# Performance work log

Measured on AMD Instinct MI355X. Metric: run time of the kernel, lower is better.

Reference implementation:

```python
import jax, jax.numpy as jnp
import numpy as np


def setup_inputs() -> dict:
    key = jax.random.key(0)
    k1, k2, k3, k4 = jax.random.split(key, 4)
    C, R = 64, 8  # channels, reduced = channels // 8
    B, D, H, W = 2, 16, 16, 16
    x = jax.random.normal(k1, (B, C, D, H, W), dtype=jnp.float32)
    # 1x1x1 Conv3d kernels are plain [out_ch, in_ch] matrices (no bias)
    Wq = jax.random.normal(k2, (R, C), dtype=jnp.float32) * (C ** -0.5)
    Wk = jax.random.normal(k3, (R, C), dtype=jnp.float32) * (C ** -0.5)
    Wv = jax.random.normal(k4, (C, C), dtype=jnp.float32) * (C ** -0.5)
    gamma = jnp.ones((1,), dtype=jnp.float32) * 0.5  # nonzero so output depends on attention
    return {"x": x, "Wq": Wq, "Wk": Wk, "Wv": Wv, "gamma": gamma}


def reference(x, Wq, Wk, Wv, gamma):
    b, c, d, h, w = x.shape
    n = d * h * w
    xf = x.astype(jnp.float32).reshape(b, c, n)        # [b, c, n]
    q = jnp.einsum('rc,bcn->bnr', Wq, xf)              # [b, n, r]
    k = jnp.einsum('rc,bcn->brn', Wk, xf)              # [b, r, n]
    scale = q.shape[-1] ** -0.5
    attn = jax.nn.softmax(jnp.einsum('bnr,brm->bnm', q, k) * scale, axis=-1)  # [b, n_q, n_k]
    v = jnp.einsum('oc,bcn->bon', Wv, xf)              # [b, c, n]
    # out = value @ attn^T : out[b,c,q] = sum_k v[b,c,k] * attn[b,q,k]
    out = jnp.einsum('bck,bqk->bcq', v, attn).reshape(b, c, d, h, w)
    return x + gamma.astype(x.dtype) * out.astype(x.dtype)
```

## Files before the change

kernel.cpp:

```cpp
#include <hip/hip_runtime.h>
#include <math.h>

#define BB 2
#define CC 64
#define NN 4096
#define SCALE 0.35355339059327373f

typedef _Float16 f16x8 __attribute__((ext_vector_type(8)));
typedef _Float16 f16x4 __attribute__((ext_vector_type(4)));
typedef float f32x4 __attribute__((ext_vector_type(4)));

__global__ __launch_bounds__(256) void proj_kernel(
    const float* __restrict__ x, const float* __restrict__ Wq,
    const float* __restrict__ Wk, const float* __restrict__ Wv,
    _Float16* __restrict__ qh, _Float16* __restrict__ kh,
    _Float16* __restrict__ vph)
{
    const int t = (int)blockIdx.x * 256 + (int)threadIdx.x;
    const int grp = t >> 13;
    const int p = t & 8191;
    const int b = p >> 12;
    const int n = p & (NN - 1);
    const float* xp = x + (size_t)b * CC * NN + n;

    float xc[CC];
#pragma unroll
    for (int c = 0; c < CC; ++c) xc[c] = xp[(size_t)c * NN];

    const float* W = (grp == 0) ? Wq : (grp == 1) ? Wk
                                     : (Wv + (size_t)(grp - 2) * 8 * CC);
    float a[8];
#pragma unroll
    for (int j = 0; j < 8; ++j) a[j] = 0.f;
#pragma unroll
    for (int c = 0; c < CC; ++c) {
        const float xv = xc[c];
#pragma unroll
        for (int j = 0; j < 8; ++j)
            a[j] = fmaf(W[j * CC + c], xv, a[j]);
    }
    if (grp == 0) {
        f16x8 o;
#pragma unroll
        for (int j = 0; j < 8; ++j) o[j] = (_Float16)(a[j] * SCALE);
        *(f16x8*)(qh + ((size_t)b * NN + n) * 8) = o;
    } else if (grp == 1) {
        f16x8 o;
#pragma unroll
        for (int j = 0; j < 8; ++j) o[j] = (_Float16)a[j];
        *(f16x8*)(kh + ((size_t)b * NN + n) * 8) = o;
    } else {
        const int c0 = (grp - 2) * 8;
        _Float16* vb = vph + ((size_t)(b * 512 + (n >> 3)) * CC + c0) * 8 + (n & 7);
#pragma unroll
        for (int j = 0; j < 8; ++j) vb[j * 8] = (_Float16)a[j];
    }
}

__global__ __launch_bounds__(512) void attn_kernel(
    const _Float16* __restrict__ qh, const _Float16* __restrict__ kh,
    const _Float16* __restrict__ vph, const float* __restrict__ x,
    const float* __restrict__ gamma, float* __restrict__ out)
{
    const int tid = (int)threadIdx.x;
    const int wid = tid >> 6;
    const int lane = tid & 63;
    const int lg = lane >> 4;
    const int lc = lane & 15;
    const int qi = (int)blockIdx.x & 255;
    const int b  = (int)blockIdx.x >> 8;
    const int q0 = qi * 16;

    __shared__ float sm_acc[8 * 64 * 17];
    __shared__ float sm_m[8][16];
    __shared__ float sm_l[8][16];

    const f16x8 zf = {};
    const f32x4 z4 = {};

    f16x8 qfrag = zf;
    if (lg == 0)
        qfrag = *(const f16x8*)(qh + ((size_t)b * NN + q0 + lc) * 8);

    float m = -1e30f, l = 0.f;
    f32x4 acc0 = z4, acc1 = z4, acc2 = z4, acc3 = z4;

    const _Float16* khb = kh + (size_t)b * NN * 8;
    const _Float16* vpb = vph + (size_t)b * 512 * CC * 8;
    const int kbase = wid * 512;

#pragma unroll 4
    for (int ch = 0; ch < 16; ++ch) {
        const int k0 = kbase + ch * 32;

        f16x8 kf0 = zf, kf1 = zf;
        if (lg == 0) {
            kf0 = *(const f16x8*)(khb + (size_t)(k0 + lc) * 8);
            kf1 = *(const f16x8*)(khb + (size_t)(k0 + 16 + lc) * 8);
        }
        const _Float16* vg = vpb + ((size_t)((k0 >> 3) + lg) * CC) * 8;
        f16x8 v0 = *(const f16x8*)(vg + (0 * 16 + lc) * 8);
        f16x8 v1 = *(const f16x8*)(vg + (1 * 16 + lc) * 8);
        f16x8 v2 = *(const f16x8*)(vg + (2 * 16 + lc) * 8);
        f16x8 v3 = *(const f16x8*)(vg + (3 * 16 + lc) * 8);

        f32x4 s0 = __builtin_amdgcn_mfma_f32_16x16x32_f16(kf0, qfrag, z4, 0, 0, 0);
        f32x4 s1 = __builtin_amdgcn_mfma_f32_16x16x32_f16(kf1, qfrag, z4, 0, 0, 0);

        float cm = fmaxf(fmaxf(fmaxf(s0[0], s0[1]), fmaxf(s0[2], s0[3])),
                         fmaxf(fmaxf(s1[0], s1[1]), fmaxf(s1[2], s1[3])));
        cm = fmaxf(cm, __shfl_xor(cm, 16));
        cm = fmaxf(cm, __shfl_xor(cm, 32));

        if (!__all(cm <= m)) {
            const float mnew = fmaxf(m, cm);
            const float alpha = __expf(m - mnew);
            m = mnew;
            l *= alpha;
            acc0 *= alpha; acc1 *= alpha; acc2 *= alpha; acc3 *= alpha;
        }

        float pr[8];
        float ls = 0.f;
#pragma unroll
        for (int v = 0; v < 4; ++v) { pr[v]     = __expf(s0[v] - m); ls += pr[v]; }
#pragma unroll
        for (int v = 0; v < 4; ++v) { pr[4 + v] = __expf(s1[v] - m); ls += pr[4 + v]; }
        ls += __shfl_xor(ls, 16);
        ls += __shfl_xor(ls, 32);
        l += ls;

        union { f16x4 h; unsigned u[2]; } P0, P1;
#pragma unroll
        for (int v = 0; v < 4; ++v) {
            P0.h[v] = (_Float16)pr[v];
            P1.h[v] = (_Float16)pr[4 + v];
        }
        const int sA = (((2 * lg) & 3) << 4) + lc;
        const int sB = (((2 * lg + 1) & 3) << 4) + lc;
        const unsigned t00 = __shfl(P0.u[0], sA), t01 = __shfl(P0.u[1], sA);
        const unsigned t10 = __shfl(P1.u[0], sA), t11 = __shfl(P1.u[1], sA);
        const unsigned u00 = __shfl(P0.u[0], sB), u01 = __shfl(P0.u[1], sB);
        const unsigned u10 = __shfl(P1.u[0], sB), u11 = __shfl(P1.u[1], sB);
        const bool hi = (lg & 2) != 0;
        union { unsigned u[4]; f16x8 v; } PF;
        PF.u[0] = hi ? t10 : t00;
        PF.u[1] = hi ? t11 : t01;
        PF.u[2] = hi ? u10 : u00;
        PF.u[3] = hi ? u11 : u01;

        acc0 = __builtin_amdgcn_mfma_f32_16x16x32_f16(v0, PF.v, acc0, 0, 0, 0);
        acc1 = __builtin_amdgcn_mfma_f32_16x16x32_f16(v1, PF.v, acc1, 0, 0, 0);
        acc2 = __builtin_amdgcn_mfma_f32_16x16x32_f16(v2, PF.v, acc2, 0, 0, 0);
        acc3 = __builtin_amdgcn_mfma_f32_16x16x32_f16(v3, PF.v, acc3, 0, 0, 0);
    }

    if (lane < 16) { sm_m[wid][lc] = m; sm_l[wid][lc] = l; }
    {
        float* sa = sm_acc + (size_t)wid * 64 * 17 + lc;
#pragma unroll
        for (int v = 0; v < 4; ++v) {
            sa[(0 * 16 + lg * 4 + v) * 17] = acc0[v];
            sa[(1 * 16 + lg * 4 + v) * 17] = acc1[v];
            sa[(2 * 16 + lg * 4 + v) * 17] = acc2[v];
            sa[(3 * 16 + lg * 4 + v) * 17] = acc3[v];
        }
    }
    __syncthreads();

    {
        const int c = tid >> 3;
        const int qb2 = (tid & 7) * 2;
        const float g = gamma[0];
#pragma unroll
        for (int dq = 0; dq < 2; ++dq) {
            const int q = qb2 + dq;
            float M = sm_m[0][q];
#pragma unroll
            for (int w = 1; w < 8; ++w) M = fmaxf(M, sm_m[w][q]);
            float L = 0.f, O = 0.f;
#pragma unroll
            for (int w = 0; w < 8; ++w) {
                const float e = __expf(sm_m[w][q] - M);
                L = fmaf(sm_l[w][q], e, L);
                O = fmaf(sm_acc[(w * 64 + c) * 17 + q], e, O);
            }
            const size_t oi = (size_t)b * CC * NN + (size_t)c * NN + q0 + q;
            out[oi] = fmaf(g, O / L, x[oi]);
        }
    }
}

extern "C" void kernel_launch(void* const* d_in, const int* in_sizes, int n_in,
                              void* d_out, int out_size, void* d_ws, size_t ws_size,
                              hipStream_t stream)
{
    const float* x     = (const float*)d_in[0];
    const float* Wq    = (const float*)d_in[1];
    const float* Wk    = (const float*)d_in[2];
    const float* Wv    = (const float*)d_in[3];
    const float* gamma = (const float*)d_in[4];
    float* out = (float*)d_out;

    char* ws = (char*)d_ws;
    _Float16* qh  = (_Float16*)ws;
    _Float16* kh  = qh + (size_t)BB * NN * 8;
    _Float16* vph = kh + (size_t)BB * NN * 8;

    hipLaunchKernelGGL(proj_kernel, dim3(320), dim3(256), 0, stream,
                       x, Wq, Wk, Wv, qh, kh, vph);
    hipLaunchKernelGGL(attn_kernel, dim3(BB * 256), dim3(512), 0, stream,
                       qh, kh, vph, x, gamma, out);
}
```

Before: 90.53 us.

## Fuse projection and attention via grid barrier, apply Wv after attention

After: 235.4 us. +160.0%, slower.

```diff
diff --git a/kernel.cpp b/kernel.cpp
--- a/kernel.cpp
+++ b/kernel.cpp
@@ -4,76 +4,89 @@
 #define BB 2
 #define CC 64
 #define NN 4096
+#define NBLK 512
 #define SCALE 0.35355339059327373f
 
 typedef _Float16 f16x8 __attribute__((ext_vector_type(8)));
 typedef _Float16 f16x4 __attribute__((ext_vector_type(4)));
 typedef float f32x4 __attribute__((ext_vector_type(4)));
 
-__global__ __launch_bounds__(256) void proj_kernel(
+union H2U { _Float16 h; unsigned short u; };
+static __device__ inline unsigned short f2h_bits(float f) {
+    H2U c; c.h = (_Float16)f; return c.u;
+}
+
+__global__ __launch_bounds__(512, 4) void fused_kernel(
     const float* __restrict__ x, const float* __restrict__ Wq,
     const float* __restrict__ Wk, const float* __restrict__ Wv,
-    _Float16* __restrict__ qh, _Float16* __restrict__ kh,
-    _Float16* __restrict__ vph)
-{
-    const int t = (int)blockIdx.x * 256 + (int)threadIdx.x;
-    const int grp = t >> 13;
-    const int p = t & 8191;
-    const int b = p >> 12;
-    const int n = p & (NN - 1);
-    const float* xp = x + (size_t)b * CC * NN + n;
-
-    float xc[CC];
-#pragma unroll
-    for (int c = 0; c < CC; ++c) xc[c] = xp[(size_t)c * NN];
-
-    const float* W = (grp == 0) ? Wq : (grp == 1) ? Wk
-                                     : (Wv + (size_t)(grp - 2) * 8 * CC);
-    float a[8];
-#pragma unroll
-    for (int j = 0; j < 8; ++j) a[j] = 0.f;
-#pragma unroll
-    for (int c = 0; c < CC; ++c) {
-        const float xv = xc[c];
-#pragma unroll
-        for (int j = 0; j < 8; ++j)
-            a[j] = fmaf(W[j * CC + c], xv, a[j]);
-    }
-    if (grp == 0) {
-        f16x8 o;
-#pragma unroll
-        for (int j = 0; j < 8; ++j) o[j] = (_Float16)(a[j] * SCALE);
-        *(f16x8*)(qh + ((size_t)b * NN + n) * 8) = o;
-    } else if (grp == 1) {
-        f16x8 o;
-#pragma unroll
-        for (int j = 0; j < 8; ++j) o[j] = (_Float16)a[j];
-        *(f16x8*)(kh + ((size_t)b * NN + n) * 8) = o;
-    } else {
-        const int c0 = (grp - 2) * 8;
-        _Float16* vb = vph + ((size_t)(b * 512 + (n >> 3)) * CC + c0) * 8 + (n & 7);
-#pragma unroll
-        for (int j = 0; j < 8; ++j) vb[j * 8] = (_Float16)a[j];
-    }
-}
-
-__global__ __launch_bounds__(512) void attn_kernel(
-    const _Float16* __restrict__ qh, const _Float16* __restrict__ kh,
-    const _Float16* __restrict__ vph, const float* __restrict__ x,
-    const float* __restrict__ gamma, float* __restrict__ out)
+    const float* __restrict__ gamma, float* __restrict__ out,
+    unsigned* __restrict__ ctr, _Float16* __restrict__ qh,
+    _Float16* __restrict__ kh, _Float16* __restrict__ xh)
 {
     const int tid = (int)threadIdx.x;
+    const int bid = (int)blockIdx.x;
+    const int gt = bid * 512 + tid;
+
+    __shared__ float sm_acc[8 * 64 * 17];
+    __shared__ float sm_m[8][16];
+    __shared__ float sm_l[8][16];
+    __shared__ float zm[64][16];
+
+    {
+        const float2 v = ((const float2*)x)[gt];
+        ushort2 h; h.x = f2h_bits(v.x); h.y = f2h_bits(v.y);
+        ((ushort2*)xh)[gt] = h;
+    }
+    if (gt < BB * NN) {
+        const int b = gt >> 12;
+        const int n = gt & (NN - 1);
+        const float* xp = x + (size_t)b * CC * NN + n;
+        float xc[CC];
+#pragma unroll
+        for (int c = 0; c < CC; ++c) xc[c] = xp[(size_t)c * NN];
+        float aq[8], ak[8];
+#pragma unroll
+        for (int r = 0; r < 8; ++r) { aq[r] = 0.f; ak[r] = 0.f; }
+#pragma unroll
+        for (int c = 0; c < CC; ++c) {
+            const float xv = xc[c];
+#pragma unroll
+            for (int r = 0; r < 8; ++r) {
+                aq[r] = fmaf(Wq[r * CC + c], xv, aq[r]);
+                ak[r] = fmaf(Wk[r * CC + c], xv, ak[r]);
+            }
+        }
+        f16x8 oq, ok;
+#pragma unroll
+        for (int r = 0; r < 8; ++r) {
+            oq[r] = (_Float16)(aq[r] * SCALE);
+            ok[r] = (_Float16)ak[r];
+        }
+        *(f16x8*)(qh + (size_t)gt * 8) = oq;
+        *(f16x8*)(kh + (size_t)gt * 8) = ok;
+    }
+
+    __threadfence();
+    __syncthreads();
+    if (tid == 0) {
+        atomicAdd(ctr, 1u);
+        int guard = 0;
+        while (__hip_atomic_load(ctr, __ATOMIC_ACQUIRE,
+                                 __HIP_MEMORY_SCOPE_AGENT) < (unsigned)NBLK &&
+               guard < (1 << 20)) {
+            __builtin_amdgcn_s_sleep(8);
+            ++guard;
+        }
+    }
+    __syncthreads();
+
     const int wid = tid >> 6;
     const int lane = tid & 63;
     const int lg = lane >> 4;
     const int lc = lane & 15;
-    const int qi = (int)blockIdx.x & 255;
-    const int b  = (int)blockIdx.x >> 8;
+    const int b  = bid & 1;
+    const int qi = bid >> 1;
     const int q0 = qi * 16;
-
-    __shared__ float sm_acc[8 * 64 * 17];
-    __shared__ float sm_m[8][16];
-    __shared__ float sm_l[8][16];
 
     const f16x8 zf = {};
     const f32x4 z4 = {};
@@ -86,7 +99,7 @@
     f32x4 acc0 = z4, acc1 = z4, acc2 = z4, acc3 = z4;
 
     const _Float16* khb = kh + (size_t)b * NN * 8;
-    const _Float16* vpb = vph + (size_t)b * 512 * CC * 8;
+    const _Float16* xhb = xh + (size_t)b * CC * NN;
     const int kbase = wid * 512;
 
 #pragma unroll 4
@@ -98,14 +111,16 @@
             kf0 = *(const f16x8*)(khb + (size_t)(k0 + lc) * 8);
             kf1 = *(const f16x8*)(khb + (size_t)(k0 + 16 + lc) * 8);
         }
-        const _Float16* vg = vpb + ((size_t)((k0 >> 3) + lg) * CC) * 8;
-        f16x8 v0 = *(const f16x8*)(vg + (0 * 16 + lc) * 8);
-        f16x8 v1 = *(const f16x8*)(vg + (1 * 16 + lc) * 8);
-        f16x8 v2 = *(const f16x8*)(vg + (2 * 16 + lc) * 8);
-        f16x8 v3 = *(const f16x8*)(vg + (3 * 16 + lc) * 8);
-
+        const _Float16* xg = xhb + (size_t)k0 + lg * 8;
+        f16x8 v0 = *(const f16x8*)(xg + (size_t)(0 * 16 + lc) * NN);
+        f16x8 v1 = *(const f16x8*)(xg + (size_t)(1 * 16 + lc) * NN);
+        f16x8 v2 = *(const f16x8*)(xg + (size_t)(2 * 16 + lc) * NN);
+        f16x8 v3 = *(const f16x8*)(xg + (size_t)(3 * 16 + lc) * NN);
+
+        __builtin_amdgcn_s_setprio(1);
         f32x4 s0 = __builtin_amdgcn_mfma_f32_16x16x32_f16(kf0, qfrag, z4, 0, 0, 0);
         f32x4 s1 = __builtin_amdgcn_mfma_f32_16x16x32_f16(kf1, qfrag, z4, 0, 0, 0);
+        __builtin_amdgcn_s_setprio(0);
 
         float cm = fmaxf(fmaxf(fmaxf(s0[0], s0[1]), fmaxf(s0[2], s0[3])),
                          fmaxf(fmaxf(s1[0], s1[1]), fmaxf(s1[2], s1[3])));
@@ -149,10 +164,12 @@
         PF.u[2] = hi ? u10 : u00;
         PF.u[3] = hi ? u11 : u01;
 
+        __builtin_amdgcn_s_setprio(1);
         acc0 = __builtin_amdgcn_mfma_f32_16x16x32_f16(v0, PF.v, acc0, 0, 0, 0);
         acc1 = __builtin_amdgcn_mfma_f32_16x16x32_f16(v1, PF.v, acc1, 0, 0, 0);
         acc2 = __builtin_amdgcn_mfma_f32_16x16x32_f16(v2, PF.v, acc2, 0, 0, 0);
         acc3 = __builtin_amdgcn_mfma_f32_16x16x32_f16(v3, PF.v, acc3, 0, 0, 0);
+        __builtin_amdgcn_s_setprio(0);
     }
 
     if (lane < 16) { sm_m[wid][lc] = m; sm_l[wid][lc] = l; }
@@ -170,11 +187,10 @@
 
     {
         const int c = tid >> 3;
-        const int qb2 = (tid & 7) * 2;
-        const float g = gamma[0];
+        const int q2 = (tid & 7) * 2;
 #pragma unroll
         for (int dq = 0; dq < 2; ++dq) {
-            const int q = qb2 + dq;
+            const int q = q2 + dq;
             float M = sm_m[0][q];
 #pragma unroll
             for (int w = 1; w < 8; ++w) M = fmaxf(M, sm_m[w][q]);
@@ -185,9 +201,26 @@
                 L = fmaf(sm_l[w][q], e, L);
                 O = fmaf(sm_acc[(w * 64 + c) * 17 + q], e, O);
             }
-            const size_t oi = (size_t)b * CC * NN + (size_t)c * NN + q0 + q;
-            out[oi] = fmaf(g, O / L, x[oi]);
-        }
+            zm[c][q] = O / L;
+        }
+    }
+    __syncthreads();
+
+    {
+        const int c = tid >> 3;
+        const int q2 = (tid & 7) * 2;
+        const float* wr = Wv + c * 64;
+        float o0 = 0.f, o1 = 0.f;
+#pragma unroll
+        for (int cc = 0; cc < 64; ++cc) {
+            const float wv = wr[cc];
+            o0 = fmaf(wv, zm[cc][q2],     o0);
+            o1 = fmaf(wv, zm[cc][q2 + 1], o1);
+        }
+        const float g = gamma[0];
+        const size_t oi = (size_t)b * CC * NN + (size_t)c * NN + q0 + q2;
+        out[oi]     = fmaf(g, o0, x[oi]);
+        out[oi + 1] = fmaf(g, o1, x[oi + 1]);
     }
 }
 
@@ -203,12 +236,12 @@
     float* out = (float*)d_out;
 
     char* ws = (char*)d_ws;
-    _Float16* qh  = (_Float16*)ws;
-    _Float16* kh  = qh + (size_t)BB * NN * 8;
-    _Float16* vph = kh + (size_t)BB * NN * 8;
-
-    hipLaunchKernelGGL(proj_kernel, dim3(320), dim3(256), 0, stream,
-                       x, Wq, Wk, Wv, qh, kh, vph);
-    hipLaunchKernelGGL(attn_kernel, dim3(BB * 256), dim3(512), 0, stream,
-                       qh, kh, vph, x, gamma, out);
+    unsigned* ctr = (unsigned*)ws;
+    _Float16* qh = (_Float16*)(ws + 256);
+    _Float16* kh = qh + (size_t)BB * NN * 8;
+    _Float16* xh = kh + (size_t)BB * NN * 8;
+
+    hipMemsetAsync(ctr, 0, 4, stream);
+    hipLaunchKernelGGL(fused_kernel, dim3(NBLK), dim3(512), 0, stream,
+                       x, Wq, Wk, Wv, gamma, out, ctr, qh, kh, xh);
 }
```

## Apply Wv after attention, widen key chunks, defer softmax rescaling

Applied to the files above, without the earlier changes.

New measurement: 87.89 us. 1.03x faster.

```diff
diff --git a/kernel.cpp b/kernel.cpp
--- a/kernel.cpp
+++ b/kernel.cpp
@@ -5,62 +5,96 @@
 #define CC 64
 #define NN 4096
 #define SCALE 0.35355339059327373f
+#define DEFER_THR 8.0f
 
 typedef _Float16 f16x8 __attribute__((ext_vector_type(8)));
 typedef _Float16 f16x4 __attribute__((ext_vector_type(4)));
 typedef float f32x4 __attribute__((ext_vector_type(4)));
+typedef float f32x4v __attribute__((ext_vector_type(4)));
 
 __global__ __launch_bounds__(256) void proj_kernel(
     const float* __restrict__ x, const float* __restrict__ Wq,
-    const float* __restrict__ Wk, const float* __restrict__ Wv,
-    _Float16* __restrict__ qh, _Float16* __restrict__ kh,
-    _Float16* __restrict__ vph)
+    const float* __restrict__ Wk, _Float16* __restrict__ qh,
+    _Float16* __restrict__ kh, _Float16* __restrict__ xp)
 {
     const int t = (int)blockIdx.x * 256 + (int)threadIdx.x;
-    const int grp = t >> 13;
-    const int p = t & 8191;
-    const int b = p >> 12;
-    const int n = p & (NN - 1);
-    const float* xp = x + (size_t)b * CC * NN + n;
-
-    float xc[CC];
-#pragma unroll
-    for (int c = 0; c < CC; ++c) xc[c] = xp[(size_t)c * NN];
-
-    const float* W = (grp == 0) ? Wq : (grp == 1) ? Wk
-                                     : (Wv + (size_t)(grp - 2) * 8 * CC);
-    float a[8];
-#pragma unroll
-    for (int j = 0; j < 8; ++j) a[j] = 0.f;
-#pragma unroll
-    for (int c = 0; c < CC; ++c) {
-        const float xv = xc[c];
-#pragma unroll
-        for (int j = 0; j < 8; ++j)
-            a[j] = fmaf(W[j * CC + c], xv, a[j]);
-    }
-    if (grp == 0) {
+
+    if (t < 16384) {
+        const int grp = t >> 13;
+        const int p = t & 8191;
+        const int b = p >> 12;
+        const int n = p & (NN - 1);
+        const float* xc0 = x + (size_t)b * CC * NN + n;
+        float xc[CC];
+#pragma unroll
+        for (int c = 0; c < CC; ++c) xc[c] = xc0[(size_t)c * NN];
+
+        const float* W = (grp == 0) ? Wq : Wk;
+        float a[8];
+#pragma unroll
+        for (int j = 0; j < 8; ++j) a[j] = 0.f;
+#pragma unroll
+        for (int c = 0; c < CC; ++c) {
+            const float xv = xc[c];
+#pragma unroll
+            for (int j = 0; j < 8; ++j)
+                a[j] = fmaf(W[j * CC + c], xv, a[j]);
+        }
         f16x8 o;
-#pragma unroll
-        for (int j = 0; j < 8; ++j) o[j] = (_Float16)(a[j] * SCALE);
-        *(f16x8*)(qh + ((size_t)b * NN + n) * 8) = o;
-    } else if (grp == 1) {
+        if (grp == 0) {
+#pragma unroll
+            for (int j = 0; j < 8; ++j) o[j] = (_Float16)(a[j] * SCALE);
+            *(f16x8*)(qh + (size_t)p * 8) = o;
+        } else {
+#pragma unroll
+            for (int j = 0; j < 8; ++j) o[j] = (_Float16)a[j];
+            *(f16x8*)(kh + (size_t)p * 8) = o;
+        }
+    } else {
+        const int pt = t - 16384;
+        const int b = pt >> 15;
+        const int g = (pt >> 6) & 511;
+        const int c = pt & 63;
+        const float* src = x + ((size_t)(b * CC + c) * NN + g * 8);
+        const float4 a0 = *(const float4*)(src);
+        const float4 a1 = *(const float4*)(src + 4);
         f16x8 o;
-#pragma unroll
-        for (int j = 0; j < 8; ++j) o[j] = (_Float16)a[j];
-        *(f16x8*)(kh + ((size_t)b * NN + n) * 8) = o;
-    } else {
-        const int c0 = (grp - 2) * 8;
-        _Float16* vb = vph + ((size_t)(b * 512 + (n >> 3)) * CC + c0) * 8 + (n & 7);
-#pragma unroll
-        for (int j = 0; j < 8; ++j) vb[j * 8] = (_Float16)a[j];
-    }
+        o[0] = (_Float16)a0.x; o[1] = (_Float16)a0.y;
+        o[2] = (_Float16)a0.z; o[3] = (_Float16)a0.w;
+        o[4] = (_Float16)a1.x; o[5] = (_Float16)a1.y;
+        o[6] = (_Float16)a1.z; o[7] = (_Float16)a1.w;
+        ((f16x8*)xp)[pt] = o;
+    }
+}
+
+static __device__ inline f16x8 make_pf(const float* p8, int lg, int lc)
+{
+    union { f16x4 h; unsigned u[2]; } P0, P1;
+#pragma unroll
+    for (int v = 0; v < 4; ++v) {
+        P0.h[v] = (_Float16)p8[v];
+        P1.h[v] = (_Float16)p8[4 + v];
+    }
+    const int sA = (((2 * lg) & 3) << 4) + lc;
+    const int sB = (((2 * lg + 1) & 3) << 4) + lc;
+    const unsigned t00 = __shfl(P0.u[0], sA), t01 = __shfl(P0.u[1], sA);
+    const unsigned t10 = __shfl(P1.u[0], sA), t11 = __shfl(P1.u[1], sA);
+    const unsigned u00 = __shfl(P0.u[0], sB), u01 = __shfl(P0.u[1], sB);
+    const unsigned u10 = __shfl(P1.u[0], sB), u11 = __shfl(P1.u[1], sB);
+    const bool hi = (lg & 2) != 0;
+    union { unsigned u[4]; f16x8 v; } PF;
+    PF.u[0] = hi ? t10 : t00;
+    PF.u[1] = hi ? t11 : t01;
+    PF.u[2] = hi ? u10 : u00;
+    PF.u[3] = hi ? u11 : u01;
+    return PF.v;
 }
 
 __global__ __launch_bounds__(512) void attn_kernel(
     const _Float16* __restrict__ qh, const _Float16* __restrict__ kh,
-    const _Float16* __restrict__ vph, const float* __restrict__ x,
-    const float* __restrict__ gamma, float* __restrict__ out)
+    const _Float16* __restrict__ xp, const float* __restrict__ x,
+    const float* __restrict__ Wv, const float* __restrict__ gamma,
+    float* __restrict__ out)
 {
     const int tid = (int)threadIdx.x;
     const int wid = tid >> 6;
@@ -74,45 +108,47 @@
     __shared__ float sm_acc[8 * 64 * 17];
     __shared__ float sm_m[8][16];
     __shared__ float sm_l[8][16];
+    __shared__ float zm[64][16];
 
     const f16x8 zf = {};
     const f32x4 z4 = {};
 
     f16x8 qfrag = zf;
     if (lg == 0)
-        qfrag = *(const f16x8*)(qh + ((size_t)b * NN + q0 + lc) * 8);
+        qfrag = *(const f16x8*)(qh + (size_t)(b * NN + q0 + lc) * 8);
 
     float m = -1e30f, l = 0.f;
     f32x4 acc0 = z4, acc1 = z4, acc2 = z4, acc3 = z4;
 
     const _Float16* khb = kh + (size_t)b * NN * 8;
-    const _Float16* vpb = vph + (size_t)b * 512 * CC * 8;
+    const _Float16* xpb = xp + (size_t)b * 512 * CC * 8;
     const int kbase = wid * 512;
 
-#pragma unroll 4
-    for (int ch = 0; ch < 16; ++ch) {
-        const int k0 = kbase + ch * 32;
-
-        f16x8 kf0 = zf, kf1 = zf;
+#pragma unroll 2
+    for (int ch = 0; ch < 8; ++ch) {
+        const int k0 = kbase + ch * 64;
+
+        f16x8 kf0 = zf, kf1 = zf, kf2 = zf, kf3 = zf;
         if (lg == 0) {
             kf0 = *(const f16x8*)(khb + (size_t)(k0 + lc) * 8);
             kf1 = *(const f16x8*)(khb + (size_t)(k0 + 16 + lc) * 8);
-        }
-        const _Float16* vg = vpb + ((size_t)((k0 >> 3) + lg) * CC) * 8;
-        f16x8 v0 = *(const f16x8*)(vg + (0 * 16 + lc) * 8);
-        f16x8 v1 = *(const f16x8*)(vg + (1 * 16 + lc) * 8);
-        f16x8 v2 = *(const f16x8*)(vg + (2 * 16 + lc) * 8);
-        f16x8 v3 = *(const f16x8*)(vg + (3 * 16 + lc) * 8);
-
+            kf2 = *(const f16x8*)(khb + (size_t)(k0 + 32 + lc) * 8);
+            kf3 = *(const f16x8*)(khb + (size_t)(k0 + 48 + lc) * 8);
+        }
         f32x4 s0 = __builtin_amdgcn_mfma_f32_16x16x32_f16(kf0, qfrag, z4, 0, 0, 0);
         f32x4 s1 = __builtin_amdgcn_mfma_f32_16x16x32_f16(kf1, qfrag, z4, 0, 0, 0);
-
-        float cm = fmaxf(fmaxf(fmaxf(s0[0], s0[1]), fmaxf(s0[2], s0[3])),
-                         fmaxf(fmaxf(s1[0], s1[1]), fmaxf(s1[2], s1[3])));
+        f32x4 s2 = __builtin_amdgcn_mfma_f32_16x16x32_f16(kf2, qfrag, z4, 0, 0, 0);
+        f32x4 s3 = __builtin_amdgcn_mfma_f32_16x16x32_f16(kf3, qfrag, z4, 0, 0, 0);
+
+        float cm = fmaxf(
+            fmaxf(fmaxf(fmaxf(s0[0], s0[1]), fmaxf(s0[2], s0[3])),
+                  fmaxf(fmaxf(s1[0], s1[1]), fmaxf(s1[2], s1[3]))),
+            fmaxf(fmaxf(fmaxf(s2[0], s2[1]), fmaxf(s2[2], s2[3])),
+                  fmaxf(fmaxf(s3[0], s3[1]), fmaxf(s3[2], s3[3]))));
         cm = fmaxf(cm, __shfl_xor(cm, 16));
         cm = fmaxf(cm, __shfl_xor(cm, 32));
 
-        if (!__all(cm <= m)) {
+        if (!__all(cm <= m + DEFER_THR)) {
             const float mnew = fmaxf(m, cm);
             const float alpha = __expf(m - mnew);
             m = mnew;
@@ -120,39 +156,44 @@
             acc0 *= alpha; acc1 *= alpha; acc2 *= alpha; acc3 *= alpha;
         }
 
-        float pr[8];
+        float pr[16];
         float ls = 0.f;
 #pragma unroll
-        for (int v = 0; v < 4; ++v) { pr[v]     = __expf(s0[v] - m); ls += pr[v]; }
-#pragma unroll
-        for (int v = 0; v < 4; ++v) { pr[4 + v] = __expf(s1[v] - m); ls += pr[4 + v]; }
+        for (int v = 0; v < 4; ++v) { pr[v]      = __expf(s0[v] - m); ls += pr[v]; }
+#pragma unroll
+        for (int v = 0; v < 4; ++v) { pr[4 + v]  = __expf(s1[v] - m); ls += pr[4 + v]; }
+#pragma unroll
+        for (int v = 0; v < 4; ++v) { pr[8 + v]  = __expf(s2[v] - m); ls += pr[8 + v]; }
+#pragma unroll
+        for (int v = 0; v < 4; ++v) { pr[12 + v] = __expf(s3[v] - m); ls += pr[12 + v]; }
         ls += __shfl_xor(ls, 16);
         ls += __shfl_xor(ls, 32);
         l += ls;
 
-        union { f16x4 h; unsigned u[2]; } P0, P1;
-#pragma unroll
-        for (int v = 0; v < 4; ++v) {
-            P0.h[v] = (_Float16)pr[v];
-            P1.h[v] = (_Float16)pr[4 + v];
-        }
-        const int sA = (((2 * lg) & 3) << 4) + lc;
-        const int sB = (((2 * lg + 1) & 3) << 4) + lc;
-        const unsigned t00 = __shfl(P0.u[0], sA), t01 = __shfl(P0.u[1], sA);
-        const unsigned t10 = __shfl(P1.u[0], sA), t11 = __shfl(P1.u[1], sA);
-        const unsigned u00 = __shfl(P0.u[0], sB), u01 = __shfl(P0.u[1], sB);
-        const unsigned u10 = __shfl(P1.u[0], sB), u11 = __shfl(P1.u[1], sB);
-        const bool hi = (lg & 2) != 0;
-        union { unsigned u[4]; f16x8 v; } PF;
-        PF.u[0] = hi ? t10 : t00;
-        PF.u[1] = hi ? t11 : t01;
-        PF.u[2] = hi ? u10 : u00;
-        PF.u[3] = hi ? u11 : u01;
-
-        acc0 = __builtin_amdgcn_mfma_f32_16x16x32_f16(v0, PF.v, acc0, 0, 0, 0);
-        acc1 = __builtin_amdgcn_mfma_f32_16x16x32_f16(v1, PF.v, acc1, 0, 0, 0);
-        acc2 = __builtin_amdgcn_mfma_f32_16x16x32_f16(v2, PF.v, acc2, 0, 0, 0);
-        acc3 = __builtin_amdgcn_mfma_f32_16x16x32_f16(v3, PF.v, acc3, 0, 0, 0);
+        {
+            const f16x8 PF = make_pf(pr, lg, lc);
+            const _Float16* vg = xpb + (size_t)((k0 >> 3) + lg) * CC * 8;
+            f16x8 v0 = *(const f16x8*)(vg + (0 * 16 + lc) * 8);
+            f16x8 v1 = *(const f16x8*)(vg + (1 * 16 + lc) * 8);
+            f16x8 v2 = *(const f16x8*)(vg + (2 * 16 + lc) * 8);
+            f16x8 v3 = *(const f16x8*)(vg + (3 * 16 + lc) * 8);
+            acc0 = __builtin_amdgcn_mfma_f32_16x16x32_f16(v0, PF, acc0, 0, 0, 0);
+            acc1 = __builtin_amdgcn_mfma_f32_16x16x32_f16(v1, PF, acc1, 0, 0, 0);
+            acc2 = __builtin_amdgcn_mfma_f32_16x16x32_f16(v2, PF, acc2, 0, 0, 0);
+            acc3 = __builtin_amdgcn_mfma_f32_16x16x32_f16(v3, PF, acc3, 0, 0, 0);
+        }
+        {
+            const f16x8 PF = make_pf(pr + 8, lg, lc);
+            const _Float16* vg = xpb + (size_t)((k0 >> 3) + 4 + lg) * CC * 8;
+            f16x8 v0 = *(const f16x8*)(vg + (0 * 16 + lc) * 8);
+            f16x8 v1 = *(const f16x8*)(vg + (1 * 16 + lc) * 8);
+            f16x8 v2 = *(const f16x8*)(vg + (2 * 16 + lc) * 8);
+            f16x8 v3 = *(const f16x8*)(vg + (3 * 16 + lc) * 8);
+            acc0 = __builtin_amdgcn_mfma_f32_16x16x32_f16(v0, PF, acc0, 0, 0, 0);
+            acc1 = __builtin_amdgcn_mfma_f32_16x16x32_f16(v1, PF, acc1, 0, 0, 0);
+            acc2 = __builtin_amdgcn_mfma_f32_16x16x32_f16(v2, PF, acc2, 0, 0, 0);
+            acc3 = __builtin_amdgcn_mfma_f32_16x16x32_f16(v3, PF, acc3, 0, 0, 0);
+        }
     }
 
     if (lane < 16) { sm_m[wid][lc] = m; sm_l[wid][lc] = l; }
@@ -170,11 +211,10 @@
 
     {
         const int c = tid >> 3;
-        const int qb2 = (tid & 7) * 2;
-        const float g = gamma[0];
+        const int q2 = (tid & 7) * 2;
 #pragma unroll
         for (int dq = 0; dq < 2; ++dq) {
-            const int q = qb2 + dq;
+            const int q = q2 + dq;
             float M = sm_m[0][q];
 #pragma unroll
             for (int w = 1; w < 8; ++w) M = fmaxf(M, sm_m[w][q]);
@@ -185,9 +225,26 @@
                 L = fmaf(sm_l[w][q], e, L);
                 O = fmaf(sm_acc[(w * 64 + c) * 17 + q], e, O);
             }
-            const size_t oi = (size_t)b * CC * NN + (size_t)c * NN + q0 + q;
-            out[oi] = fmaf(g, O / L, x[oi]);
-        }
+            zm[c][q] = O / L;
+        }
+    }
+    __syncthreads();
+
+    {
+        const int c = tid >> 3;
+        const int q2 = (tid & 7) * 2;
+        const float* wr = Wv + c * 64;
+        float o0 = 0.f, o1 = 0.f;
+#pragma unroll
+        for (int cc = 0; cc < 64; ++cc) {
+            const float wv = wr[cc];
+            o0 = fmaf(wv, zm[cc][q2],     o0);
+            o1 = fmaf(wv, zm[cc][q2 + 1], o1);
+        }
+        const float g = gamma[0];
+        const size_t oi = (size_t)b * CC * NN + (size_t)c * NN + q0 + q2;
+        out[oi]     = fmaf(g, o0, x[oi]);
+        out[oi + 1] = fmaf(g, o1, x[oi + 1]);
     }
 }
 
@@ -203,12 +260,12 @@
     float* out = (float*)d_out;
 
     char* ws = (char*)d_ws;
-    _Float16* qh  = (_Float16*)ws;
-    _Float16* kh  = qh + (size_t)BB * NN * 8;
-    _Float16* vph = kh + (size_t)BB * NN * 8;
+    _Float16* qh = (_Float16*)ws;
+    _Float16* kh = qh + (size_t)BB * NN * 8;
+    _Float16* xp = kh + (size_t)BB * NN * 8;
 
     hipLaunchKernelGGL(proj_kernel, dim3(320), dim3(256), 0, stream,
-                       x, Wq, Wk, Wv, qh, kh, vph);
+                       x, Wq, Wk, qh, kh, xp);
     hipLaunchKernelGGL(attn_kernel, dim3(BB * 256), dim3(512), 0, stream,
-                       qh, kh, vph, x, gamma, out);
-}
+                       qh, kh, xp, x, Wv, gamma, out);
+}
```
